# Optimization experiments

Hardware: AMD Instinct MI355X
Metric: run time of the kernel (lower is better)

The kernel has to match this reference:

```python
import jax, jax.numpy as jnp
import numpy as np

NBITS = 4  # asymmetric fake-quant

def fake_quant_asym(w, bit):
    # mask of nonzero weights (zeros stay zero after quantization)
    mask = (w != 0).astype(w.dtype)
    max_ = jnp.max(w)
    min_ = jnp.min(w)
    alpha = max_ - min_
    beta = min_
    step = (2 ** bit) - 1
    ws = (w - beta) / alpha
    R = jnp.round(step * ws) / step
    wq = alpha * R + beta
    return wq * mask

def setup_inputs() -> dict:
    key = jax.random.key(0)
    k1, k2, k3 = jax.random.split(key, 3)
    m, n = 1024, 1024
    std = np.sqrt(2.0 / (m + n))
    x = jax.random.normal(k1, (16384, m), dtype=jnp.float32)
    weight = jax.random.normal(k2, (n, m), dtype=jnp.float32) * std
    bias = jax.random.normal(k3, (n,), dtype=jnp.float32) * 0.01
    return {"x": x, "weight": weight, "bias": bias}

def reference(x, weight, bias):
    wq = fake_quant_asym(weight, NBITS)
    # F.linear: y = x @ W^T + b
    return jnp.einsum('tm,nm->tn', x, wq) + bias
```

## Files before the change

### kernel.cpp

```cpp
#include <hip/hip_runtime.h>

#define M_DIM 16384
#define N_DIM 1024
#define K_DIM 1024

typedef short v8s __attribute__((ext_vector_type(8)));
typedef float v4f __attribute__((ext_vector_type(4)));

__device__ __forceinline__ unsigned short f2bf(float f) {
  unsigned u = __float_as_uint(f);
  unsigned r = (u + 0x7FFFu + ((u >> 16) & 1u)) >> 16;
  return (unsigned short)r;
}

__device__ __forceinline__ void gload16(const void* g, void* l) {
  __builtin_amdgcn_global_load_lds(
      (const __attribute__((address_space(1))) void*)g,
      (__attribute__((address_space(3))) void*)l, 16, 0, 0);
}

#define DSR(dst, addr, off) \
  asm volatile("ds_read_b128 %0, %1 offset:" off : "=v"(dst) : "v"(addr))

__global__ void wminmax_part(const float* __restrict__ w, float* __restrict__ part) {
  int tid = blockIdx.x * 256 + threadIdx.x;
  float mx = -3.402823466e38f, mn = 3.402823466e38f;
  for (int i = tid; i < N_DIM * K_DIM; i += 256 * 256) {
    float v = w[i];
    mx = fmaxf(mx, v);
    mn = fminf(mn, v);
  }
  #pragma unroll
  for (int o = 32; o > 0; o >>= 1) {
    mx = fmaxf(mx, __shfl_down(mx, o));
    mn = fminf(mn, __shfl_down(mn, o));
  }
  __shared__ float smx[4], smn[4];
  int lane = threadIdx.x & 63, wv = threadIdx.x >> 6;
  if (lane == 0) { smx[wv] = mx; smn[wv] = mn; }
  __syncthreads();
  if (threadIdx.x == 0) {
    mx = fmaxf(fmaxf(smx[0], smx[1]), fmaxf(smx[2], smx[3]));
    mn = fminf(fminf(smn[0], smn[1]), fminf(smn[2], smn[3]));
    part[blockIdx.x] = mx;
    part[256 + blockIdx.x] = mn;
  }
}

__global__ void wminmax_final(const float* __restrict__ part, float* __restrict__ mm) {
  float mx = part[threadIdx.x];
  float mn = part[256 + threadIdx.x];
  #pragma unroll
  for (int o = 32; o > 0; o >>= 1) {
    mx = fmaxf(mx, __shfl_down(mx, o));
    mn = fminf(mn, __shfl_down(mn, o));
  }
  __shared__ float smx[4], smn[4];
  int lane = threadIdx.x & 63, wv = threadIdx.x >> 6;
  if (lane == 0) { smx[wv] = mx; smn[wv] = mn; }
  __syncthreads();
  if (threadIdx.x == 0) {
    mm[0] = fmaxf(fmaxf(smx[0], smx[1]), fmaxf(smx[2], smx[3]));
    mm[1] = fminf(fminf(smn[0], smn[1]), fminf(smn[2], smn[3]));
  }
}

__global__ void quant_kernel(const float* __restrict__ w, const float* __restrict__ mm,
                             unsigned short* __restrict__ wq) {
  const float mx = mm[0], mn = mm[1];
  const float alpha = mx - mn, beta = mn;
  int i = (blockIdx.x * 256 + threadIdx.x) * 4;
  float4 v = *(const float4*)(w + i);
  float f[4] = {v.x, v.y, v.z, v.w};
  ushort4 o;
  unsigned short ov[4];
  #pragma unroll
  for (int j = 0; j < 4; j++) {
    float s = (f[j] - beta) / alpha;
    float R = rintf(15.0f * s) / 15.0f;
    float q = alpha * R + beta;
    if (f[j] == 0.0f) q = 0.0f;
    ov[j] = f2bf(q);
  }
  o.x = ov[0]; o.y = ov[1]; o.z = ov[2]; o.w = ov[3];
  *(ushort4*)(wq + i) = o;
}

__global__ void conv_kernel(const float* __restrict__ x, unsigned short* __restrict__ xbf) {
  int i = (blockIdx.x * 256 + threadIdx.x) * 8;
  float4 a = *(const float4*)(x + i);
  float4 b = *(const float4*)(x + i + 4);
  union { v8s v; unsigned short u[8]; } o;
  o.u[0] = f2bf(a.x); o.u[1] = f2bf(a.y); o.u[2] = f2bf(a.z); o.u[3] = f2bf(a.w);
  o.u[4] = f2bf(b.x); o.u[5] = f2bf(b.y); o.u[6] = f2bf(b.z); o.u[7] = f2bf(b.w);
  *(v8s*)(xbf + i) = o.v;
}

__global__ __launch_bounds__(512, 2) void gemm8p_kernel(
    const unsigned short* __restrict__ xbf, const unsigned short* __restrict__ wq,
    const float* __restrict__ bias, float* __restrict__ out) {
  __shared__ __attribute__((aligned(16))) unsigned short As[2][2][2][128][32];
  __shared__ __attribute__((aligned(16))) unsigned short Bs[2][2][2][128][32];

  const int tid = threadIdx.x;
  const int lane = tid & 63;
  const int wv = tid >> 6;
  const int wr = wv >> 2;
  const int wc = wv & 3;
  const int bm = blockIdx.x;
  const int bn = blockIdx.y;

  const int srow = wv * 16 + (lane >> 2);
  const int ssw = ((lane & 3) ^ ((lane >> 3) & 3)) * 8;
  const unsigned short* aS = xbf + (size_t)(bm * 256 + srow) * K_DIM + ssw;
  const unsigned short* bS = wq + (size_t)(bn * 256 + srow) * K_DIM + ssw;

  const int frow = lane & 15;
  const int kc = lane >> 4;
  const int fswB = (kc ^ ((frow >> 1) & 3)) * 16;
  const unsigned ldsA0 =
      (unsigned)(unsigned long long)(__attribute__((address_space(3))) unsigned short*)&As[0][0][0][0][0];
  const unsigned ldsB0 =
      (unsigned)(unsigned long long)(__attribute__((address_space(3))) unsigned short*)&Bs[0][0][0][0][0];
  const unsigned aLane = ldsA0 + wr * 16384u + (unsigned)(frow * 64 + fswB);
  const unsigned bLane = ldsB0 + (wc >> 1) * 16384u + (wc & 1) * 4096u + (unsigned)(frow * 64 + fswB);

  v4f acc[8][4];
  #pragma unroll
  for (int m = 0; m < 8; m++)
    #pragma unroll
    for (int n = 0; n < 4; n++) acc[m][n] = (v4f)(0.0f);

  v8s af[8], bf0, bf1;

#define GATE(N) do { \
    asm volatile("s_waitcnt vmcnt(" #N ")" ::: "memory"); \
    __builtin_amdgcn_s_barrier(); \
  } while (0)

#define MMX(NH) do { \
    asm volatile("s_waitcnt lgkmcnt(0)" ::: "memory"); \
    __builtin_amdgcn_sched_barrier(0); \
    __builtin_amdgcn_s_setprio(1); \
    _Pragma("unroll") \
    for (int m_ = 0; m_ < 8; m_++) { \
      acc[m_][2*(NH)]   = __builtin_amdgcn_mfma_f32_16x16x32_bf16(af[m_], bf0, acc[m_][2*(NH)], 0, 0, 0); \
      acc[m_][2*(NH)+1] = __builtin_amdgcn_mfma_f32_16x16x32_bf16(af[m_], bf1, acc[m_][2*(NH)+1], 0, 0, 0); \
    } \
    __builtin_amdgcn_s_setprio(0); \
  } while (0)

#define KSHALF(BUF, KS, ktv, STG) do { \
    const unsigned aP = aLane + (BUF) * 32768u + (KS) * 8192u; \
    const unsigned bP = bLane + (BUF) * 32768u + (KS) * 8192u; \
    DSR(af[0], aP, "0");    DSR(af[1], aP, "1024"); \
    DSR(af[2], aP, "2048"); DSR(af[3], aP, "3072"); \
    DSR(af[4], aP, "4096"); DSR(af[5], aP, "5120"); \
    DSR(af[6], aP, "6144"); DSR(af[7], aP, "7168"); \
    DSR(bf0, bP, "0");      DSR(bf1, bP, "1024"); \
    if (STG) { \
      gload16(aS + (size_t)(ktv + 1) * 64 + (KS) * 32, &As[(BUF) ^ 1][0][KS][wv * 16][0]); \
      gload16(aS + 131072 + (size_t)(ktv + 1) * 64 + (KS) * 32, &As[(BUF) ^ 1][1][KS][wv * 16][0]); \
    } \
    MMX(0); \
    DSR(bf0, bP, "2048");   DSR(bf1, bP, "3072"); \
    if (STG) { \
      gload16(bS + (size_t)(ktv + 1) * 64 + (KS) * 32, &Bs[(BUF) ^ 1][0][KS][wv * 16][0]); \
      gload16(bS + 131072 + (size_t)(ktv + 1) * 64 + (KS) * 32, &Bs[(BUF) ^ 1][1][KS][wv * 16][0]); \
    } \
    MMX(1); \
  } while (0)

#define KTILE(BUF, ktv, STG, GBN) do { \
    GATE(4); \
    KSHALF(BUF, 0, ktv, STG); \
    GATE(GBN); \
    KSHALF(BUF, 1, ktv, STG); \
  } while (0)

  gload16(aS, &As[0][0][0][wv * 16][0]);
  gload16(aS + 131072, &As[0][1][0][wv * 16][0]);
  gload16(bS, &Bs[0][0][0][wv * 16][0]);
  gload16(bS + 131072, &Bs[0][1][0][wv * 16][0]);
  gload16(aS + 32, &As[0][0][1][wv * 16][0]);
  gload16(aS + 131072 + 32, &As[0][1][1][wv * 16][0]);
  gload16(bS + 32, &Bs[0][0][1][wv * 16][0]);
  gload16(bS + 131072 + 32, &Bs[0][1][1][wv * 16][0]);

  #pragma unroll 1
  for (int kt2 = 0; kt2 < 7; kt2++) {
    const int kt = kt2 * 2;
    KTILE(0, kt, 1, 4);
    KTILE(1, kt + 1, 1, 4);
  }
  KTILE(0, 14, 1, 4);
  KTILE(1, 15, 0, 0);

#undef KTILE
#undef KSHALF
#undef MMX
#undef GATE

  const int colbase = bn * 256 + wc * 64;
  const int rowbase = bm * 256 + wr * 128;
  #pragma unroll
  for (int n = 0; n < 4; n++) {
    const int col = colbase + n * 16 + (lane & 15);
    const float bv = bias[col];
    #pragma unroll
    for (int m = 0; m < 8; m++) {
      const int row0 = rowbase + m * 16 + (lane >> 4) * 4;
      #pragma unroll
      for (int r = 0; r < 4; r++)
        out[(size_t)(row0 + r) * N_DIM + col] = acc[m][n][r] + bv;
    }
  }
}

__global__ __launch_bounds__(256) void gemm_kernel(
    const float* __restrict__ x, const unsigned short* __restrict__ wq,
    const float* __restrict__ bias, float* __restrict__ out) {
  __shared__ __attribute__((aligned(16))) unsigned short As[2][128][32];
  __shared__ __attribute__((aligned(16))) unsigned short Bs[2][128][32];

  const int tid = threadIdx.x;
  const int lane = tid & 63;
  const int wv = tid >> 6;
  const int wr = wv >> 1, wc = wv & 1;
  const int bm = blockIdx.x, bn = blockIdx.y;

  const int arow = tid >> 1;
  const int acol = (tid & 1) << 4;
  const float* aptr = x + (size_t)(bm * 128 + arow) * K_DIM + acol;
  const int fA = (arow >> 1) & 3;
  const int ac0 = (tid & 1) * 2;
  const int aw0 = ((ac0) ^ fA) * 8;
  const int aw1 = ((ac0 + 1) ^ fA) * 8;

  const int brow0 = wv * 32 + (lane >> 2);
  const int bsrcc = (lane & 3) ^ ((lane >> 3) & 3);
  const unsigned short* bptr0 = wq + (size_t)(bn * 128 + brow0) * K_DIM + bsrcc * 8;
  const unsigned short* bptr1 = bptr0 + (size_t)16 * K_DIM;

  v4f acc[4][4];
  #pragma unroll
  for (int i = 0; i < 4; i++)
    #pragma unroll
    for (int j = 0; j < 4; j++) acc[i][j] = (v4f)(0.0f);

  const int frow = lane & 15;
  const int fkc = lane >> 4;
  const int fsw = (fkc ^ ((frow >> 1) & 3)) * 8;

  float4 areg[4];
  #pragma unroll
  for (int j = 0; j < 4; j++) areg[j] = *(const float4*)(aptr + j * 4);

  {
    const float* f = (const float*)areg;
    union { v8s v; unsigned short u[8]; } cv0, cv1;
    #pragma unroll
    for (int i = 0; i < 8; i++) { cv0.u[i] = f2bf(f[i]); cv1.u[i] = f2bf(f[i + 8]); }
    *(v8s*)&As[0][arow][aw0] = cv0.v;
    *(v8s*)&As[0][arow][aw1] = cv1.v;
    gload16(bptr0, &Bs[0][wv * 32][0]);
    gload16(bptr1, &Bs[0][wv * 32 + 16][0]);
  }
  #pragma unroll
  for (int j = 0; j < 4; j++) areg[j] = *(const float4*)(aptr + 32 + j * 4);
  __syncthreads();

  for (int kt = 0; kt < K_DIM / 32; ++kt) {
    const int cur = kt & 1, nxt = cur ^ 1;
    if (kt + 1 < K_DIM / 32) {
      const float* f = (const float*)areg;
      union { v8s v; unsigned short u[8]; } cv0, cv1;
      #pragma unroll
      for (int i = 0; i < 8; i++) { cv0.u[i] = f2bf(f[i]); cv1.u[i] = f2bf(f[i + 8]); }
      *(v8s*)&As[nxt][arow][aw0] = cv0.v;
      *(v8s*)&As[nxt][arow][aw1] = cv1.v;
      gload16(bptr0 + (size_t)(kt + 1) * 32, &Bs[nxt][wv * 32][0]);
      gload16(bptr1 + (size_t)(kt + 1) * 32, &Bs[nxt][wv * 32 + 16][0]);
      if (kt + 2 < K_DIM / 32) {
        const float* ap = aptr + (kt + 2) * 32;
        #pragma unroll
        for (int j = 0; j < 4; j++) areg[j] = *(const float4*)(ap + j * 4);
      }
    }
    v8s af[4], bf[4];
    #pragma unroll
    for (int m = 0; m < 4; m++)
      af[m] = *(const v8s*)&As[cur][wr * 64 + m * 16 + frow][fsw];
    #pragma unroll
    for (int n = 0; n < 4; n++)
      bf[n] = *(const v8s*)&Bs[cur][wc * 64 + n * 16 + frow][fsw];
    #pragma unroll
    for (int m = 0; m < 4; m++)
      #pragma unroll
      for (int n = 0; n < 4; n++)
        acc[m][n] = __builtin_amdgcn_mfma_f32_16x16x32_bf16(af[m], bf[n], acc[m][n], 0, 0, 0);
    __syncthreads();
  }

  const int colbase = bn * 128 + wc * 64;
  const int rowbase = bm * 128 + wr * 64;
  #pragma unroll
  for (int n = 0; n < 4; n++) {
    const int col = colbase + n * 16 + (lane & 15);
    const float bv = bias[col];
    #pragma unroll
    for (int m = 0; m < 4; m++) {
      const int row0 = rowbase + m * 16 + (lane >> 4) * 4;
      #pragma unroll
      for (int r = 0; r < 4; r++)
        out[(size_t)(row0 + r) * N_DIM + col] = acc[m][n][r] + bv;
    }
  }
}

extern "C" void kernel_launch(void* const* d_in, const int* in_sizes, int n_in,
                              void* d_out, int out_size, void* d_ws, size_t ws_size,
                              hipStream_t stream) {
  const float* x = (const float*)d_in[0];
  const float* wt = (const float*)d_in[1];
  const float* bias = (const float*)d_in[2];
  float* out = (float*)d_out;

  float* part = (float*)d_ws;
  float* mm = part + 512;
  unsigned short* wqbuf = (unsigned short*)((char*)d_ws + 4096);
  unsigned short* xbf = (unsigned short*)((char*)d_ws + 4096 + 2 * 1024 * 1024);
  const size_t need = 4096 + 2ull * 1024 * 1024 + 2ull * M_DIM * K_DIM;

  wminmax_part<<<256, 256, 0, stream>>>(wt, part);
  wminmax_final<<<1, 256, 0, stream>>>(part, mm);
  quant_kernel<<<1024, 256, 0, stream>>>(wt, mm, wqbuf);

  if (ws_size >= need) {
    conv_kernel<<<M_DIM * K_DIM / (8 * 256), 256, 0, stream>>>(x, xbf);
    dim3 grid(M_DIM / 256, N_DIM / 256);
    gemm8p_kernel<<<grid, 512, 0, stream>>>(xbf, wqbuf, bias, out);
  } else {
    dim3 grid(M_DIM / 128, N_DIM / 128);
    gemm_kernel<<<grid, 256, 0, stream>>>(x, wqbuf, bias, out);
  }
}
```

Measured before the change: 70.31 us.

## Replace double-buffered GEMM pipeline with four-slot LDS ring and 4x4 MFMA phases

```diff
diff --git a/kernel.cpp b/kernel.cpp
--- a/kernel.cpp
+++ b/kernel.cpp
@@ -96,11 +96,11 @@
   *(v8s*)(xbf + i) = o.v;
 }
 
-__global__ __launch_bounds__(512, 2) void gemm8p_kernel(
+__global__ __launch_bounds__(512, 2) void gemm_ring(
     const unsigned short* __restrict__ xbf, const unsigned short* __restrict__ wq,
     const float* __restrict__ bias, float* __restrict__ out) {
-  __shared__ __attribute__((aligned(16))) unsigned short As[2][2][2][128][32];
-  __shared__ __attribute__((aligned(16))) unsigned short Bs[2][2][2][128][32];
+  __shared__ __attribute__((aligned(16))) unsigned short As[4][256][32];
+  __shared__ __attribute__((aligned(16))) unsigned short Bs[4][256][32];
 
   const int tid = threadIdx.x;
   const int lane = tid & 63;
@@ -110,20 +110,19 @@
   const int bm = blockIdx.x;
   const int bn = blockIdx.y;
 
-  const int srow = wv * 16 + (lane >> 2);
+  const int srow = wv * 32 + (lane >> 2);
   const int ssw = ((lane & 3) ^ ((lane >> 3) & 3)) * 8;
   const unsigned short* aS = xbf + (size_t)(bm * 256 + srow) * K_DIM + ssw;
   const unsigned short* bS = wq + (size_t)(bn * 256 + srow) * K_DIM + ssw;
 
   const int frow = lane & 15;
-  const int kc = lane >> 4;
-  const int fswB = (kc ^ ((frow >> 1) & 3)) * 16;
+  const int fsw = ((lane >> 4) ^ ((frow >> 1) & 3)) * 8;
   const unsigned ldsA0 =
-      (unsigned)(unsigned long long)(__attribute__((address_space(3))) unsigned short*)&As[0][0][0][0][0];
+      (unsigned)(unsigned long long)(__attribute__((address_space(3))) unsigned short*)&As[0][0][0];
   const unsigned ldsB0 =
-      (unsigned)(unsigned long long)(__attribute__((address_space(3))) unsigned short*)&Bs[0][0][0][0][0];
-  const unsigned aLane = ldsA0 + wr * 16384u + (unsigned)(frow * 64 + fswB);
-  const unsigned bLane = ldsB0 + (wc >> 1) * 16384u + (wc & 1) * 4096u + (unsigned)(frow * 64 + fswB);
+      (unsigned)(unsigned long long)(__attribute__((address_space(3))) unsigned short*)&Bs[0][0][0];
+  const unsigned aLane = ldsA0 + (unsigned)((wr * 128 + frow) * 32 + fsw) * 2u;
+  const unsigned bLane = ldsB0 + (unsigned)((wc * 64 + frow) * 32 + fsw) * 2u;
 
   v4f acc[8][4];
   #pragma unroll
@@ -131,75 +130,78 @@
     #pragma unroll
     for (int n = 0; n < 4; n++) acc[m][n] = (v4f)(0.0f);
 
-  v8s af[8], bf0, bf1;
-
-#define GATE(N) do { \
-    asm volatile("s_waitcnt vmcnt(" #N ")" ::: "memory"); \
+  v8s af[4], bf[4];
+
+#define STAGE_A(H_) do { \
+    gload16(aS + (size_t)(H_) * 32, &As[(H_) & 3][wv * 32][0]); \
+    gload16(aS + (size_t)(H_) * 32 + 16 * K_DIM, &As[(H_) & 3][wv * 32 + 16][0]); \
+  } while (0)
+#define STAGE_B(H_) do { \
+    gload16(bS + (size_t)(H_) * 32, &Bs[(H_) & 3][wv * 32][0]); \
+    gload16(bS + (size_t)(H_) * 32 + 16 * K_DIM, &Bs[(H_) & 3][wv * 32 + 16][0]); \
+  } while (0)
+
+#define MM16(MH_) do { \
+    _Pragma("unroll") \
+    for (int i_ = 0; i_ < 4; i_++) \
+      _Pragma("unroll") \
+      for (int n_ = 0; n_ < 4; n_++) \
+        acc[(MH_) * 4 + i_][n_] = __builtin_amdgcn_mfma_f32_16x16x32_bf16( \
+            af[i_], bf[n_], acc[(MH_) * 4 + i_][n_], 0, 0, 0); \
+  } while (0)
+
+#define PH0(H_, STG_) do { \
+    const unsigned aP = aLane + ((H_) & 3) * 16384u; \
+    const unsigned bP = bLane + ((H_) & 3) * 16384u; \
+    DSR(af[0], aP, "0");    DSR(af[1], aP, "1024"); \
+    DSR(af[2], aP, "2048"); DSR(af[3], aP, "3072"); \
+    DSR(bf[0], bP, "0");    DSR(bf[1], bP, "1024"); \
+    DSR(bf[2], bP, "2048"); DSR(bf[3], bP, "3072"); \
+    if (STG_) STAGE_A((H_) + 3); \
     __builtin_amdgcn_s_barrier(); \
-  } while (0)
-
-#define MMX(NH) do { \
     asm volatile("s_waitcnt lgkmcnt(0)" ::: "memory"); \
     __builtin_amdgcn_sched_barrier(0); \
     __builtin_amdgcn_s_setprio(1); \
-    _Pragma("unroll") \
-    for (int m_ = 0; m_ < 8; m_++) { \
-      acc[m_][2*(NH)]   = __builtin_amdgcn_mfma_f32_16x16x32_bf16(af[m_], bf0, acc[m_][2*(NH)], 0, 0, 0); \
-      acc[m_][2*(NH)+1] = __builtin_amdgcn_mfma_f32_16x16x32_bf16(af[m_], bf1, acc[m_][2*(NH)+1], 0, 0, 0); \
-    } \
+    MM16(0); \
     __builtin_amdgcn_s_setprio(0); \
-  } while (0)
-
-#define KSHALF(BUF, KS, ktv, STG) do { \
-    const unsigned aP = aLane + (BUF) * 32768u + (KS) * 8192u; \
-    const unsigned bP = bLane + (BUF) * 32768u + (KS) * 8192u; \
+    __builtin_amdgcn_s_barrier(); \
+  } while (0)
+
+#define PH1(H_, STG_, GATE_) do { \
+    const unsigned aP = aLane + ((H_) & 3) * 16384u + 4096u; \
     DSR(af[0], aP, "0");    DSR(af[1], aP, "1024"); \
     DSR(af[2], aP, "2048"); DSR(af[3], aP, "3072"); \
-    DSR(af[4], aP, "4096"); DSR(af[5], aP, "5120"); \
-    DSR(af[6], aP, "6144"); DSR(af[7], aP, "7168"); \
-    DSR(bf0, bP, "0");      DSR(bf1, bP, "1024"); \
-    if (STG) { \
-      gload16(aS + (size_t)(ktv + 1) * 64 + (KS) * 32, &As[(BUF) ^ 1][0][KS][wv * 16][0]); \
-      gload16(aS + 131072 + (size_t)(ktv + 1) * 64 + (KS) * 32, &As[(BUF) ^ 1][1][KS][wv * 16][0]); \
-    } \
-    MMX(0); \
-    DSR(bf0, bP, "2048");   DSR(bf1, bP, "3072"); \
-    if (STG) { \
-      gload16(bS + (size_t)(ktv + 1) * 64 + (KS) * 32, &Bs[(BUF) ^ 1][0][KS][wv * 16][0]); \
-      gload16(bS + 131072 + (size_t)(ktv + 1) * 64 + (KS) * 32, &Bs[(BUF) ^ 1][1][KS][wv * 16][0]); \
-    } \
-    MMX(1); \
-  } while (0)
-
-#define KTILE(BUF, ktv, STG, GBN) do { \
-    GATE(4); \
-    KSHALF(BUF, 0, ktv, STG); \
-    GATE(GBN); \
-    KSHALF(BUF, 1, ktv, STG); \
-  } while (0)
-
-  gload16(aS, &As[0][0][0][wv * 16][0]);
-  gload16(aS + 131072, &As[0][1][0][wv * 16][0]);
-  gload16(bS, &Bs[0][0][0][wv * 16][0]);
-  gload16(bS + 131072, &Bs[0][1][0][wv * 16][0]);
-  gload16(aS + 32, &As[0][0][1][wv * 16][0]);
-  gload16(aS + 131072 + 32, &As[0][1][1][wv * 16][0]);
-  gload16(bS + 32, &Bs[0][0][1][wv * 16][0]);
-  gload16(bS + 131072 + 32, &Bs[0][1][1][wv * 16][0]);
+    if (STG_) STAGE_B((H_) + 3); \
+    __builtin_amdgcn_s_barrier(); \
+    asm volatile("s_waitcnt lgkmcnt(0)" ::: "memory"); \
+    __builtin_amdgcn_sched_barrier(0); \
+    __builtin_amdgcn_s_setprio(1); \
+    MM16(1); \
+    __builtin_amdgcn_s_setprio(0); \
+    asm volatile("s_waitcnt vmcnt(" GATE_ ")" ::: "memory"); \
+    __builtin_amdgcn_s_barrier(); \
+  } while (0)
+
+  STAGE_A(0); STAGE_B(0);
+  STAGE_A(1); STAGE_B(1);
+  STAGE_A(2); STAGE_B(2);
+  asm volatile("s_waitcnt vmcnt(8)" ::: "memory");
+  __builtin_amdgcn_s_barrier();
 
   #pragma unroll 1
-  for (int kt2 = 0; kt2 < 7; kt2++) {
-    const int kt = kt2 * 2;
-    KTILE(0, kt, 1, 4);
-    KTILE(1, kt + 1, 1, 4);
-  }
-  KTILE(0, 14, 1, 4);
-  KTILE(1, 15, 0, 0);
-
-#undef KTILE
-#undef KSHALF
-#undef MMX
-#undef GATE
+  for (int h = 0; h < 29; ++h) {
+    PH0(h, 1);
+    PH1(h, 1, "8");
+  }
+  PH0(29, 0); PH1(29, 0, "4");
+  PH0(30, 0); PH1(30, 0, "0");
+  PH0(31, 0); PH1(31, 0, "0");
+
+#undef PH0
+#undef PH1
+#undef MM16
+#undef STAGE_A
+#undef STAGE_B
 
   const int colbase = bn * 256 + wc * 64;
   const int rowbase = bm * 256 + wr * 128;
@@ -339,7 +341,7 @@
   if (ws_size >= need) {
     conv_kernel<<<M_DIM * K_DIM / (8 * 256), 256, 0, stream>>>(x, xbf);
     dim3 grid(M_DIM / 256, N_DIM / 256);
-    gemm8p_kernel<<<grid, 512, 0, stream>>>(xbf, wqbuf, bias, out);
+    gemm_ring<<<grid, 512, 0, stream>>>(xbf, wqbuf, bias, out);
   } else {
     dim3 grid(M_DIM / 128, N_DIM / 128);
     gemm_kernel<<<grid, 256, 0, stream>>>(x, wqbuf, bias, out);
```

Result: no change. 71.57 us (+1.8%).
